# Kernel tuning notes

Measured on AMD Instinct MI355X. Metric: run time of the kernel, lower is better.

## Reference

```python
import jax, jax.numpy as jnp
import numpy as np

HEADS = 16
EMB_DIM = 1024
MODEL_DIM = 1024
HEAD_DIM = EMB_DIM // HEADS
N, SEQ = 4, 1024


def setup_inputs() -> dict:
    key = jax.random.key(0)
    ks = jax.random.split(key, 9)
    s = 1.0 / np.sqrt(EMB_DIM)
    return {
        "query_inputs": jax.random.normal(ks[0], (N, SEQ, EMB_DIM), jnp.float32),
        "key_inputs": jax.random.normal(ks[1], (N, SEQ, EMB_DIM), jnp.float32),
        "value_inputs": jax.random.normal(ks[2], (N, SEQ, EMB_DIM), jnp.float32),
        "Wq": jax.random.normal(ks[3], (MODEL_DIM, EMB_DIM), jnp.float32) * s,
        "bq": jax.random.normal(ks[4], (MODEL_DIM,), jnp.float32) * s,
        "Wk": jax.random.normal(ks[5], (MODEL_DIM, EMB_DIM), jnp.float32) * s,
        "bk": jax.random.normal(ks[6], (MODEL_DIM,), jnp.float32) * s,
        "Wv": jax.random.normal(ks[7], (MODEL_DIM, EMB_DIM), jnp.float32) * s,
        "bv": jax.random.normal(ks[8], (MODEL_DIM,), jnp.float32) * s,
    }


def reference(query_inputs, key_inputs, value_inputs, Wq, bq, Wk, bk, Wv, bv):
    n = query_inputs.shape[0]
    qi = query_inputs.reshape(n, -1, query_inputs.shape[-1])
    ki = key_inputs.reshape(n, -1, key_inputs.shape[-1])
    vi = value_inputs.reshape(n, -1, value_inputs.shape[-1])
    q = qi @ Wq.T + bq  # (n, L, model_dim)
    k = ki @ Wk.T + bk
    v = vi @ Wv.T + bv
    L = q.shape[1]
    # Faithful to original (q/v swapped role): 'values'<-q, 'queries'<-v
    values = q.reshape(n, L, HEADS, HEAD_DIM)
    keys = k.reshape(n, L, HEADS, HEAD_DIM)
    queries = v.reshape(n, L, HEADS, HEAD_DIM)
    energy = jnp.einsum('nqhd,nkhd->nhqk', queries, keys)
    attention = jax.nn.softmax(energy / jnp.sqrt(jnp.float32(EMB_DIM)), axis=3)
    out = jnp.einsum('nhql,nlhd->nqhd', attention, values).reshape(n, L, HEADS * HEAD_DIM)
    return out
```

## Files before the change

### kernel.cpp

```cpp
#include <hip/hip_runtime.h>


typedef unsigned short u16;
typedef __attribute__((ext_vector_type(8))) short bf16x8;
typedef __attribute__((ext_vector_type(4))) float f32x4;

#define S_LEN 1024
#define EMB 1024
#define HEADS 16
#define HD 64

__device__ __forceinline__ u16 f2bf(float f) {
    unsigned int u = __float_as_uint(f);
    u = (u + 0x7fffu + ((u >> 16) & 1u)) >> 16;
    return (u16)u;
}

typedef const __attribute__((address_space(1))) unsigned glob_u32;
typedef __attribute__((address_space(3))) unsigned lds_u32;
__device__ __forceinline__ void gld16(const u16* g, u16* l) {
    __builtin_amdgcn_global_load_lds((glob_u32*)g, (lds_u32*)l, 16, 0, 0);
}

struct CvtArgs {
    const float* src[6];
    u16* dst[6];
};

__global__ __launch_bounds__(256) void cvt_f32_bf16(CvtArgs a)
{
    const long total = (3L << 20) + (3L << 18);
    for (long i = (long)blockIdx.x * 256 + threadIdx.x; i < total;
         i += (long)gridDim.x * 256) {
        int arr, off;
        if (i < (3L << 20)) { arr = (int)(i >> 20); off = (int)(i & ((1 << 20) - 1)); }
        else { long j = i - (3L << 20); arr = 3 + (int)(j >> 18); off = (int)(j & ((1 << 18) - 1)); }
        float4 v = reinterpret_cast<const float4*>(a.src[arr])[off];
        ushort4 o; o.x = f2bf(v.x); o.y = f2bf(v.y); o.z = f2bf(v.z); o.w = f2bf(v.w);
        reinterpret_cast<ushort4*>(a.dst[arr])[off] = o;
    }
}

__global__ __launch_bounds__(512) void qkv_gemm_bf16(
    const u16* __restrict__ Xq, const u16* __restrict__ Xk, const u16* __restrict__ Xv,
    const u16* __restrict__ Wq, const u16* __restrict__ Wk, const u16* __restrict__ Wv,
    const float* __restrict__ Bq, const float* __restrict__ Bk, const float* __restrict__ Bv,
    u16* __restrict__ vt, u16* __restrict__ katt, u16* __restrict__ qatt)
{
    const int proj = blockIdx.z;
    const u16* X  = (proj == 0) ? Xq : (proj == 1) ? Xk : Xv;
    const u16* W  = (proj == 0) ? Wq : (proj == 1) ? Wk : Wv;
    const float* Bp = (proj == 0) ? Bq : (proj == 1) ? Bk : Bv;

    const int gm0 = blockIdx.x * 128;
    const int gn0 = blockIdx.y * 128;
    const int tid  = threadIdx.x;
    const int lane = tid & 63;
    const int wave = tid >> 6;
    const int wm = wave >> 2, wn = wave & 3;
    const int l15 = lane & 15, l4 = lane >> 4;

    __shared__ u16 As[3][128 * 32];
    __shared__ u16 Bs[3][128 * 32];

    f32x4 acc[4][2];
    #pragma unroll
    for (int i = 0; i < 4; ++i)
        #pragma unroll
        for (int j = 0; j < 2; ++j) { f32x4 z = {0.f,0.f,0.f,0.f}; acc[i][j] = z; }

    const int rr  = tid >> 2;
    const int ccg = (tid & 3) ^ ((tid >> 3) & 3);
    const u16* gA = X + (size_t)(gm0 + rr) * EMB + ccg * 8;
    const u16* gB = W + (size_t)(gn0 + rr) * EMB + ccg * 8;

    auto stage = [&](int buf, int ktile) {
        const int k0 = ktile * 32;
        gld16(gA + k0, &As[buf][wave * 512]);
        gld16(gB + k0, &Bs[buf][wave * 512]);
    };

    const int swz = (l15 >> 1) & 3;
    auto compute = [&](int buf) {
        const u16* A = &As[buf][0];
        const u16* B = &Bs[buf][0];
        bf16x8 af[4], bfr[2];
        #pragma unroll
        for (int m = 0; m < 4; ++m)
            af[m] = *reinterpret_cast<const bf16x8*>(&A[(wm * 64 + m * 16 + l15) * 32 + ((l4 ^ swz) * 8)]);
        #pragma unroll
        for (int n = 0; n < 2; ++n)
            bfr[n] = *reinterpret_cast<const bf16x8*>(&B[(wn * 32 + n * 16 + l15) * 32 + ((l4 ^ swz) * 8)]);
        __builtin_amdgcn_s_setprio(1);
        #pragma unroll
        for (int m = 0; m < 4; ++m)
            #pragma unroll
            for (int n = 0; n < 2; ++n)
                acc[m][n] = __builtin_amdgcn_mfma_f32_16x16x32_bf16(af[m], bfr[n], acc[m][n], 0, 0, 0);
        __builtin_amdgcn_s_setprio(0);
    };

    stage(0, 0);
    stage(1, 1);

    #pragma unroll 1
    for (int base = 0; base < 30; base += 3) {
        asm volatile("s_waitcnt vmcnt(2)" ::: "memory");
        __builtin_amdgcn_s_barrier();
        stage(2, base + 2);
        compute(0);
        asm volatile("s_waitcnt vmcnt(2)" ::: "memory");
        __builtin_amdgcn_s_barrier();
        stage(0, base + 3);
        compute(1);
        asm volatile("s_waitcnt vmcnt(2)" ::: "memory");
        __builtin_amdgcn_s_barrier();
        stage(1, base + 4);
        compute(2);
    }
    asm volatile("s_waitcnt vmcnt(2)" ::: "memory");
    __builtin_amdgcn_s_barrier();
    compute(0);
    asm volatile("s_waitcnt vmcnt(0)" ::: "memory");
    __builtin_amdgcn_s_barrier();
    compute(1);

    #pragma unroll
    for (int n = 0; n < 2; ++n) {
        const int col = gn0 + wn * 32 + n * 16 + l15;
        const float bias = Bp[col];
        const int h = col >> 6, d = col & 63;
        #pragma unroll
        for (int m = 0; m < 4; ++m) {
            #pragma unroll
            for (int r = 0; r < 4; ++r) {
                const int rowg = gm0 + wm * 64 + m * 16 + l4 * 4 + r;
                const int nb = rowg >> 10, s = rowg & 1023;
                const u16 val = f2bf(acc[m][n][r] + bias);
                const int nh = nb * HEADS + h;
                if (proj == 0)       vt  [((size_t)nh * HD + d) * S_LEN + s] = val;
                else if (proj == 1)  katt[((size_t)nh * S_LEN + s) * HD + d] = val;
                else                 qatt[((size_t)nh * S_LEN + s) * HD + d] = val;
            }
        }
    }
}

__global__ __launch_bounds__(256) void qkv_gemm_f32(
    const float* __restrict__ Xq, const float* __restrict__ Xk, const float* __restrict__ Xv,
    const float* __restrict__ Wq, const float* __restrict__ Wk, const float* __restrict__ Wv,
    const float* __restrict__ Bq, const float* __restrict__ Bk, const float* __restrict__ Bv,
    u16* __restrict__ vt, u16* __restrict__ katt, u16* __restrict__ qatt)
{
    const int proj = blockIdx.z;
    const float* X = (proj == 0) ? Xq : (proj == 1) ? Xk : Xv;
    const float* W = (proj == 0) ? Wq : (proj == 1) ? Wk : Wv;
    const float* Bp = (proj == 0) ? Bq : (proj == 1) ? Bk : Bv;

    const int gm0 = blockIdx.x * 128;
    const int gn0 = blockIdx.y * 128;
    const int tid  = threadIdx.x;
    const int lane = tid & 63;
    const int wave = tid >> 6;
    const int wm = wave >> 1, wn = wave & 1;
    const int l15 = lane & 15, l4 = lane >> 4;

    __shared__ u16 As[128 * 40];
    __shared__ u16 Bs[128 * 40];

    f32x4 acc[4][4];
    #pragma unroll
    for (int i = 0; i < 4; ++i)
        #pragma unroll
        for (int j = 0; j < 4; ++j) { f32x4 z = {0.f,0.f,0.f,0.f}; acc[i][j] = z; }

    const int srow = tid >> 3;
    const int skc  = (tid & 7) * 4;

    for (int kt = 0; kt < 32; ++kt) {
        const int k0 = kt * 32;
        #pragma unroll
        for (int p = 0; p < 4; ++p) {
            const int row = p * 32 + srow;
            float4 a = *reinterpret_cast<const float4*>(&X[(size_t)(gm0 + row) * EMB + k0 + skc]);
            float4 b = *reinterpret_cast<const float4*>(&W[(size_t)(gn0 + row) * EMB + k0 + skc]);
            ushort4 ua; ua.x = f2bf(a.x); ua.y = f2bf(a.y); ua.z = f2bf(a.z); ua.w = f2bf(a.w);
            ushort4 ub; ub.x = f2bf(b.x); ub.y = f2bf(b.y); ub.z = f2bf(b.z); ub.w = f2bf(b.w);
            *reinterpret_cast<ushort4*>(&As[row * 40 + skc]) = ua;
            *reinterpret_cast<ushort4*>(&Bs[row * 40 + skc]) = ub;
        }
        __syncthreads();

        bf16x8 af[4], bfr[4];
        #pragma unroll
        for (int m = 0; m < 4; ++m)
            af[m] = *reinterpret_cast<const bf16x8*>(&As[(wm * 64 + m * 16 + l15) * 40 + l4 * 8]);
        #pragma unroll
        for (int n = 0; n < 4; ++n)
            bfr[n] = *reinterpret_cast<const bf16x8*>(&Bs[(wn * 64 + n * 16 + l15) * 40 + l4 * 8]);

        #pragma unroll
        for (int m = 0; m < 4; ++m)
            #pragma unroll
            for (int n = 0; n < 4; ++n)
                acc[m][n] = __builtin_amdgcn_mfma_f32_16x16x32_bf16(af[m], bfr[n], acc[m][n], 0, 0, 0);
        __syncthreads();
    }

    #pragma unroll
    for (int n = 0; n < 4; ++n) {
        const int col = gn0 + wn * 64 + n * 16 + l15;
        const float bias = Bp[col];
        const int h = col >> 6, d = col & 63;
        #pragma unroll
        for (int m = 0; m < 4; ++m) {
            #pragma unroll
            for (int r = 0; r < 4; ++r) {
                const int rowg = gm0 + wm * 64 + m * 16 + l4 * 4 + r;
                const int nb = rowg >> 10, s = rowg & 1023;
                const u16 val = f2bf(acc[m][n][r] + bias);
                const int nh = nb * HEADS + h;
                if (proj == 0)       vt  [((size_t)nh * HD + d) * S_LEN + s] = val;
                else if (proj == 1)  katt[((size_t)nh * S_LEN + s) * HD + d] = val;
                else                 qatt[((size_t)nh * S_LEN + s) * HD + d] = val;
            }
        }
    }
}

__global__ __launch_bounds__(256) void attn_kernel(
    const u16* __restrict__ qatt, const u16* __restrict__ katt,
    const u16* __restrict__ vt, float* __restrict__ out)
{
    const int qb = blockIdx.x;
    const int nh = blockIdx.y;
    const int tid  = threadIdx.x;
    const int lane = tid & 63;
    const int wave = tid >> 6;
    const int l15 = lane & 15, l4 = lane >> 4;
    const int q0 = qb * 64;
    const int waveQ = wave * 16;

    __shared__ u16 Ks[2][64 * 64];
    __shared__ u16 Vs[2][64 * 64];
    __shared__ u16 Ps[4 * 16 * 72];

    const size_t qbase = (size_t)nh * S_LEN * HD + (size_t)(q0 + waveQ + l15) * HD;
    const bf16x8 qf0 = *reinterpret_cast<const bf16x8*>(&qatt[qbase + l4 * 8]);
    const bf16x8 qf1 = *reinterpret_cast<const bf16x8*>(&qatt[qbase + 32 + l4 * 8]);

    const int r8  = lane >> 3;
    const int ccg = (lane & 7) ^ r8;
    const int row0 = wave * 8 + r8;
    const int row1 = 32 + row0;
    const u16* gK = katt + (size_t)nh * S_LEN * HD;
    const u16* gV = vt   + (size_t)nh * HD * S_LEN;
    const u16* gK0 = gK + (size_t)row0 * HD + ccg * 8;
    const u16* gK1 = gK + (size_t)row1 * HD + ccg * 8;
    const u16* gV0 = gV + (size_t)row0 * S_LEN + ccg * 8;
    const u16* gV1 = gV + (size_t)row1 * S_LEN + ccg * 8;

    f32x4 accO[4];
    #pragma unroll
    for (int i = 0; i < 4; ++i) { f32x4 z = {0.f,0.f,0.f,0.f}; accO[i] = z; }
    float lsum[4] = {0.f, 0.f, 0.f, 0.f};
    const float scale = 0.03125f;

    {
        u16* kb = &Ks[0][0] + wave * 512;
        u16* vb = &Vs[0][0] + wave * 512;
        gld16(gK0, kb);          gld16(gK1, kb + 2048);
        gld16(gV0, vb);          gld16(gV1, vb + 2048);
    }
    __syncthreads();

    for (int kt = 0; kt < 16; ++kt) {
        const int cur = kt & 1;
        if (kt < 15) {
            const size_t kOff = (size_t)(kt + 1) * 64 * HD;
            const size_t vOff = (size_t)(kt + 1) * 64;
            u16* kb = &Ks[cur ^ 1][0] + wave * 512;
            u16* vb = &Vs[cur ^ 1][0] + wave * 512;
            gld16(gK0 + kOff, kb);       gld16(gK1 + kOff, kb + 2048);
            gld16(gV0 + vOff, vb);       gld16(gV1 + vOff, vb + 2048);
        }

        char* KsB = reinterpret_cast<char*>(&Ks[cur][0]);
        char* VsB = reinterpret_cast<char*>(&Vs[cur][0]);

        float pvals[4][4];
        #pragma unroll
        for (int kb = 0; kb < 4; ++kb) {
            const int krow = kb * 16 + l15;
            const int sw = krow & 7;
            bf16x8 kf0 = *reinterpret_cast<const bf16x8*>(KsB + krow * 128 + ((l4 ^ sw) << 4));
            bf16x8 kf1 = *reinterpret_cast<const bf16x8*>(KsB + krow * 128 + (((l4 + 4) ^ sw) << 4));
            f32x4 sacc = {0.f, 0.f, 0.f, 0.f};
            __builtin_amdgcn_s_setprio(1);
            sacc = __builtin_amdgcn_mfma_f32_16x16x32_bf16(qf0, kf0, sacc, 0, 0, 0);
            sacc = __builtin_amdgcn_mfma_f32_16x16x32_bf16(qf1, kf1, sacc, 0, 0, 0);
            __builtin_amdgcn_s_setprio(0);
            #pragma unroll
            for (int r = 0; r < 4; ++r) {
                const float pv = __expf(sacc[r] * scale);
                pvals[kb][r] = pv;
                lsum[r] += pv;
            }
        }

        u16* pw = &Ps[wave * 16 * 72];
        #pragma unroll
        for (int r = 0; r < 4; ++r) {
            const int prow = l4 * 4 + r;
            #pragma unroll
            for (int kb = 0; kb < 4; ++kb)
                pw[prow * 72 + kb * 16 + l15] = f2bf(pvals[kb][r]);
        }
        asm volatile("s_waitcnt lgkmcnt(0)" ::: "memory");
        __builtin_amdgcn_sched_barrier(0);

        const u16* pr = &Ps[wave * 16 * 72 + l15 * 72];
        const bf16x8 pf0 = *reinterpret_cast<const bf16x8*>(&pr[l4 * 8]);
        const bf16x8 pf1 = *reinterpret_cast<const bf16x8*>(&pr[32 + l4 * 8]);

        __builtin_amdgcn_s_setprio(1);
        #pragma unroll
        for (int db = 0; db < 4; ++db) {
            const int vrow = db * 16 + l15;
            const int sw = vrow & 7;
            bf16x8 vf0 = *reinterpret_cast<const bf16x8*>(VsB + vrow * 128 + ((l4 ^ sw) << 4));
            bf16x8 vf1 = *reinterpret_cast<const bf16x8*>(VsB + vrow * 128 + (((l4 + 4) ^ sw) << 4));
            accO[db] = __builtin_amdgcn_mfma_f32_16x16x32_bf16(pf0, vf0, accO[db], 0, 0, 0);
            accO[db] = __builtin_amdgcn_mfma_f32_16x16x32_bf16(pf1, vf1, accO[db], 0, 0, 0);
        }
        __builtin_amdgcn_s_setprio(0);
        __syncthreads();
    }

    #pragma unroll
    for (int r = 0; r < 4; ++r) {
        float s = lsum[r];
        #pragma unroll
        for (int msk = 1; msk < 16; msk <<= 1) s += __shfl_xor(s, msk);
        lsum[r] = 1.0f / s;
    }

    const int n = nh >> 4, h = nh & 15;
    #pragma unroll
    for (int db = 0; db < 4; ++db) {
        const int d = h * 64 + db * 16 + l15;
        #pragma unroll
        for (int r = 0; r < 4; ++r) {
            const int s = q0 + waveQ + l4 * 4 + r;
            out[(size_t)n * S_LEN * EMB + (size_t)s * EMB + d] = accO[db][r] * lsum[r];
        }
    }
}

extern "C" void kernel_launch(void* const* d_in, const int* in_sizes, int n_in,
                              void* d_out, int out_size, void* d_ws, size_t ws_size,
                              hipStream_t stream)
{
    const float* Xq = (const float*)d_in[0];
    const float* Xk = (const float*)d_in[1];
    const float* Xv = (const float*)d_in[2];
    const float* Wq = (const float*)d_in[3];
    const float* bq = (const float*)d_in[4];
    const float* Wk = (const float*)d_in[5];
    const float* bk = (const float*)d_in[6];
    const float* Wv = (const float*)d_in[7];
    const float* bv = (const float*)d_in[8];
    float* out = (float*)d_out;

    const size_t M4 = (size_t)4 * 1024 * 1024;
    const size_t M1 = (size_t)1024 * 1024;

    u16* vt   = (u16*)d_ws;
    u16* katt = vt + M4;
    u16* qatt = katt + M4;

    const size_t need = (3 * M4 + 3 * M4 + 3 * M1) * sizeof(u16);

    if (ws_size >= need) {
        u16* Xqb = qatt + M4;
        u16* Xkb = Xqb + M4;
        u16* Xvb = Xkb + M4;
        u16* Wqb = Xvb + M4;
        u16* Wkb = Wqb + M1;
        u16* Wvb = Wkb + M1;

        CvtArgs ca;
        ca.src[0] = Xq; ca.src[1] = Xk; ca.src[2] = Xv;
        ca.src[3] = Wq; ca.src[4] = Wk; ca.src[5] = Wv;
        ca.dst[0] = Xqb; ca.dst[1] = Xkb; ca.dst[2] = Xvb;
        ca.dst[3] = Wqb; ca.dst[4] = Wkb; ca.dst[5] = Wvb;
        cvt_f32_bf16<<<2048, 256, 0, stream>>>(ca);

        qkv_gemm_bf16<<<dim3(32, 8, 3), 512, 0, stream>>>(
            Xqb, Xkb, Xvb, Wqb, Wkb, Wvb, bq, bk, bv, vt, katt, qatt);
    } else {
        qkv_gemm_f32<<<dim3(32, 8, 3), 256, 0, stream>>>(
            Xq, Xk, Xv, Wq, Wk, Wv, bq, bk, bv, vt, katt, qatt);
    }

    attn_kernel<<<dim3(16, 64), 256, 0, stream>>>(qatt, katt, vt, out);
}
```

Measured before the change: 196.2 us.

## Keep softmax probabilities in registers via transposed QK MFMA and lane shuffles

Swaps the MFMA operand order so the score tile comes out transposed, with each lane holding one query row's values. The probabilities are then packed to bf16 with v_cvt_pk_bf16_f32 and redistributed into the PV A-operand layout using cross-lane shuffles, replacing the LDS store, wait and reload of the P tile. Row sums collapse to a single per-lane scalar, reduced with two xor shuffles at the end. This trades LDS traffic and its wait for 16 ds_bpermute-style shuffles per tile plus selects, and the inline asm conversion must agree with the previous rounding.

```diff
diff --git a/kernel.cpp b/kernel.cpp
--- a/kernel.cpp
+++ b/kernel.cpp
@@ -243,7 +243,6 @@
 
     __shared__ u16 Ks[2][64 * 64];
     __shared__ u16 Vs[2][64 * 64];
-    __shared__ u16 Ps[4 * 16 * 72];
 
     const size_t qbase = (size_t)nh * S_LEN * HD + (size_t)(q0 + waveQ + l15) * HD;
     const bf16x8 qf0 = *reinterpret_cast<const bf16x8*>(&qatt[qbase + l4 * 8]);
@@ -263,7 +262,7 @@
     f32x4 accO[4];
     #pragma unroll
     for (int i = 0; i < 4; ++i) { f32x4 z = {0.f,0.f,0.f,0.f}; accO[i] = z; }
-    float lsum[4] = {0.f, 0.f, 0.f, 0.f};
+    float lsum = 0.f;
     const float scale = 0.03125f;
 
     {
@@ -273,6 +272,10 @@
         gld16(gV0, vb);          gld16(gV1, vb + 2048);
     }
     __syncthreads();
+
+    const int srcA = l15 + ((l4 & 1) << 5);
+    const int srcB = srcA + 16;
+    const bool lo = (l4 < 2);
 
     for (int kt = 0; kt < 16; ++kt) {
         const int cur = kt & 1;
@@ -288,7 +291,7 @@
         char* KsB = reinterpret_cast<char*>(&Ks[cur][0]);
         char* VsB = reinterpret_cast<char*>(&Vs[cur][0]);
 
-        float pvals[4][4];
+        float pv[4][4];
         #pragma unroll
         for (int kb = 0; kb < 4; ++kb) {
             const int krow = kb * 16 + l15;
@@ -297,31 +300,43 @@
             bf16x8 kf1 = *reinterpret_cast<const bf16x8*>(KsB + krow * 128 + (((l4 + 4) ^ sw) << 4));
             f32x4 sacc = {0.f, 0.f, 0.f, 0.f};
             __builtin_amdgcn_s_setprio(1);
-            sacc = __builtin_amdgcn_mfma_f32_16x16x32_bf16(qf0, kf0, sacc, 0, 0, 0);
-            sacc = __builtin_amdgcn_mfma_f32_16x16x32_bf16(qf1, kf1, sacc, 0, 0, 0);
+            sacc = __builtin_amdgcn_mfma_f32_16x16x32_bf16(kf0, qf0, sacc, 0, 0, 0);
+            sacc = __builtin_amdgcn_mfma_f32_16x16x32_bf16(kf1, qf1, sacc, 0, 0, 0);
             __builtin_amdgcn_s_setprio(0);
             #pragma unroll
             for (int r = 0; r < 4; ++r) {
-                const float pv = __expf(sacc[r] * scale);
-                pvals[kb][r] = pv;
-                lsum[r] += pv;
+                const float p = __expf(sacc[r] * scale);
+                pv[kb][r] = p;
+                lsum += p;
             }
         }
 
-        u16* pw = &Ps[wave * 16 * 72];
-        #pragma unroll
-        for (int r = 0; r < 4; ++r) {
-            const int prow = l4 * 4 + r;
-            #pragma unroll
-            for (int kb = 0; kb < 4; ++kb)
-                pw[prow * 72 + kb * 16 + l15] = f2bf(pvals[kb][r]);
-        }
-        asm volatile("s_waitcnt lgkmcnt(0)" ::: "memory");
-        __builtin_amdgcn_sched_barrier(0);
-
-        const u16* pr = &Ps[wave * 16 * 72 + l15 * 72];
-        const bf16x8 pf0 = *reinterpret_cast<const bf16x8*>(&pr[l4 * 8]);
-        const bf16x8 pf1 = *reinterpret_cast<const bf16x8*>(&pr[32 + l4 * 8]);
+        unsigned pk0l, pk0h, pk1l, pk1h, pk2l, pk2h, pk3l, pk3h;
+        asm("v_cvt_pk_bf16_f32 %0, %1, %2" : "=v"(pk0l) : "v"(pv[0][0]), "v"(pv[0][1]));
+        asm("v_cvt_pk_bf16_f32 %0, %1, %2" : "=v"(pk0h) : "v"(pv[0][2]), "v"(pv[0][3]));
+        asm("v_cvt_pk_bf16_f32 %0, %1, %2" : "=v"(pk1l) : "v"(pv[1][0]), "v"(pv[1][1]));
+        asm("v_cvt_pk_bf16_f32 %0, %1, %2" : "=v"(pk1h) : "v"(pv[1][2]), "v"(pv[1][3]));
+        asm("v_cvt_pk_bf16_f32 %0, %1, %2" : "=v"(pk2l) : "v"(pv[2][0]), "v"(pv[2][1]));
+        asm("v_cvt_pk_bf16_f32 %0, %1, %2" : "=v"(pk2h) : "v"(pv[2][2]), "v"(pv[2][3]));
+        asm("v_cvt_pk_bf16_f32 %0, %1, %2" : "=v"(pk3l) : "v"(pv[3][0]), "v"(pv[3][1]));
+        asm("v_cvt_pk_bf16_f32 %0, %1, %2" : "=v"(pk3h) : "v"(pv[3][2]), "v"(pv[3][3]));
+
+        int a, b;
+        int w0, w1, w2, w3, x0, x1, x2, x3;
+        a = __shfl((int)pk0l, srcA); b = __shfl((int)pk1l, srcA); w0 = lo ? a : b;
+        a = __shfl((int)pk0h, srcA); b = __shfl((int)pk1h, srcA); w1 = lo ? a : b;
+        a = __shfl((int)pk0l, srcB); b = __shfl((int)pk1l, srcB); w2 = lo ? a : b;
+        a = __shfl((int)pk0h, srcB); b = __shfl((int)pk1h, srcB); w3 = lo ? a : b;
+        a = __shfl((int)pk2l, srcA); b = __shfl((int)pk3l, srcA); x0 = lo ? a : b;
+        a = __shfl((int)pk2h, srcA); b = __shfl((int)pk3h, srcA); x1 = lo ? a : b;
+        a = __shfl((int)pk2l, srcB); b = __shfl((int)pk3l, srcB); x2 = lo ? a : b;
+        a = __shfl((int)pk2h, srcB); b = __shfl((int)pk3h, srcB); x3 = lo ? a : b;
+
+        union { int4 i; bf16x8 v; } u0, u1;
+        u0.i = make_int4(w0, w1, w2, w3);
+        u1.i = make_int4(x0, x1, x2, x3);
+        const bf16x8 pf0 = u0.v;
+        const bf16x8 pf1 = u1.v;
 
         __builtin_amdgcn_s_setprio(1);
         #pragma unroll
@@ -337,13 +352,14 @@
         __syncthreads();
     }
 
-    #pragma unroll
-    for (int r = 0; r < 4; ++r) {
-        float s = lsum[r];
-        #pragma unroll
-        for (int msk = 1; msk < 16; msk <<= 1) s += __shfl_xor(s, msk);
-        lsum[r] = 1.0f / s;
-    }
+    lsum += __shfl_xor(lsum, 16);
+    lsum += __shfl_xor(lsum, 32);
+    const float inv = 1.0f / lsum;
+
+    float dr[4];
+    #pragma unroll
+    for (int r = 0; r < 4; ++r)
+        dr[r] = __shfl(inv, l4 * 4 + r);
 
     const int n = nh >> 4, h = nh & 15;
     #pragma unroll
@@ -352,7 +368,7 @@
         #pragma unroll
         for (int r = 0; r < 4; ++r) {
             const int s = q0 + waveQ + l4 * 4 + r;
-            out[(size_t)n * S_LEN * EMB + (size_t)s * EMB + d] = accO[db][r] * lsum[r];
+            out[(size_t)n * S_LEN * EMB + (size_t)s * EMB + d] = accO[db][r] * dr[r];
         }
     }
 }
```

New measurement: 189.6 us. -3.4%, faster.
